# Optimization experiments

Measured on AMD Instinct MI355X. Metric: run time of the kernel, lower is better.

Reference implementation:

```python
import jax, jax.numpy as jnp
import numpy as np

NUM_USER = 200000
NUM_ITEM = 100000
DIM_E = 64
N_LAYERS = 3
N_INTER = 1000000  # raw sampled interactions (deduped below)
BATCH = 8192
EDGE_DROP = 0.5    # torch uses np.random.random()*1.0; fixed here for determinism
TGT_DROP = 0.5     # self.dropout


def _xavier_uniform(key, shape):
    fan_in, fan_out = shape[0], shape[1]
    b = np.sqrt(6.0 / (fan_in + fan_out)).astype(np.float32)
    return jax.random.uniform(key, shape, jnp.float32, -b, b)


def setup_inputs() -> dict:
    rng = np.random.default_rng(0)
    u = rng.integers(0, NUM_USER, N_INTER).astype(np.int64)
    it = rng.integers(0, NUM_ITEM, N_INTER).astype(np.int64)
    pair = np.unique(u * NUM_ITEM + it)  # dedupe like the dok_matrix update
    u, it = pair // NUM_ITEM, pair % NUM_ITEM
    # symmetric bipartite adjacency A over N = U + I nodes
    rows = np.concatenate([u, it + NUM_USER])
    cols = np.concatenate([it + NUM_USER, u])
    n_nodes = NUM_USER + NUM_ITEM
    deg = np.bincount(rows, minlength=n_nodes).astype(np.float32) + 1e-7
    dinv = np.power(deg, -0.5)
    vals = (dinv[rows] * dinv[cols]).astype(np.float32)  # D^-1/2 A D^-1/2

    key = jax.random.key(0)
    k1, k2, k3, k4 = jax.random.split(key, 4)
    return {
        "user_emb": _xavier_uniform(k1, (NUM_USER, DIM_E)),
        "item_emb": _xavier_uniform(k2, (NUM_ITEM, DIM_E)),
        "adj_vals": jnp.asarray(vals),
        "adj_rows": jnp.asarray(rows),
        "adj_cols": jnp.asarray(cols),
        "users": jax.random.randint(k3, (BATCH,), 0, NUM_USER),
        "items": jax.random.randint(k4, (BATCH,), 0, NUM_ITEM),
    }


def _spmm(rows, cols, vals, x, n_nodes):
    # out[r] = sum_e vals[e] * x[cols[e]] for rows[e] == r  (COO SpMM)
    return jax.ops.segment_sum(vals[:, None] * x[cols], rows, num_segments=n_nodes)


def reference(user_emb, item_emb, adj_vals, adj_rows, adj_cols, users, items):
    n_nodes = user_emb.shape[0] + item_emb.shape[0]
    kd = jax.random.key(1234)
    ke, ku, ki = jax.random.split(kd, 3)

    # sparse edge dropout: floor(1-rate + U[0,1)) keep mask, rescale by 1/(1-rate)
    keep = jnp.floor(1.0 - EDGE_DROP + jax.random.uniform(ke, adj_vals.shape))
    vals = adj_vals * keep * (1.0 / (1.0 - EDGE_DROP))

    x = jnp.concatenate([user_emb, item_emb], axis=0)  # [N, D]
    acc = x
    for _ in range(N_LAYERS):
        x = _spmm(adj_rows, adj_cols, vals, x, n_nodes)
        acc = acc + x
    all_emb = acc / (N_LAYERS + 1)  # mean over the stacked hops

    u_all = all_emb[:user_emb.shape[0]]
    i_all = all_emb[user_emb.shape[0]:]
    u_online = u_all[users]
    i_online = i_all[items]

    # targets: detached copies with standard dropout
    u_t = jax.lax.stop_gradient(u_online)
    i_t = jax.lax.stop_gradient(i_online)
    um = jax.random.bernoulli(ku, 1.0 - TGT_DROP, u_t.shape)
    im = jax.random.bernoulli(ki, 1.0 - TGT_DROP, i_t.shape)
    u_target = jnp.where(um, u_t / (1.0 - TGT_DROP), 0.0)
    i_target = jnp.where(im, i_t / (1.0 - TGT_DROP), 0.0)
    return (u_online, u_target, i_online, i_target)
```

## Files before the change

kernel.cpp:

```cpp
#include <hip/hip_runtime.h>
#include <stdint.h>

__host__ __device__ inline void tf2x32(uint32_t k0, uint32_t k1,
                                       uint32_t x0, uint32_t x1,
                                       uint32_t& o0, uint32_t& o1) {
  const uint32_t ks2 = k0 ^ k1 ^ 0x1BD11BDAu;
  x0 += k0; x1 += k1;
#define TFR(r) { x0 += x1; x1 = (x1 << (r)) | (x1 >> (32 - (r))); x1 ^= x0; }
  TFR(13) TFR(15) TFR(26) TFR(6)
  x0 += k1;  x1 += ks2 + 1u;
  TFR(17) TFR(29) TFR(16) TFR(24)
  x0 += ks2; x1 += k0 + 2u;
  TFR(13) TFR(15) TFR(26) TFR(6)
  x0 += k0;  x1 += k1 + 3u;
  TFR(17) TFR(29) TFR(16) TFR(24)
  x0 += k1;  x1 += ks2 + 4u;
  TFR(13) TFR(15) TFR(26) TFR(6)
  x0 += ks2; x1 += k0 + 5u;
#undef TFR
  o0 = x0; o1 = x1;
}

__host__ __device__ inline uint32_t bits32(uint32_t k0, uint32_t k1, uint32_t idx) {
  uint32_t a, b;
  tf2x32(k0, k1, 0u, idx, a, b);
  return a ^ b;
}

__device__ inline bool edge_kept(uint32_t k0, uint32_t k1, uint32_t e) {
  return (bits32(k0, k1, e) >> 31) != 0u;
}

__device__ inline float bf_lo(uint32_t u) { return __uint_as_float(u << 16); }
__device__ inline float bf_hi(uint32_t u) { return __uint_as_float(u & 0xffff0000u); }
__device__ inline uint32_t bf_pack(float a, float b) {
  uint32_t lo = (__float_as_uint(a) + 0x8000u) >> 16;
  uint32_t hi = (__float_as_uint(b) + 0x8000u) & 0xffff0000u;
  return hi | lo;
}

__device__ inline void fma8_f32(float a[8], float v, const float4& x0, const float4& x1) {
  a[0] = fmaf(v, x0.x, a[0]); a[1] = fmaf(v, x0.y, a[1]);
  a[2] = fmaf(v, x0.z, a[2]); a[3] = fmaf(v, x0.w, a[3]);
  a[4] = fmaf(v, x1.x, a[4]); a[5] = fmaf(v, x1.y, a[5]);
  a[6] = fmaf(v, x1.z, a[6]); a[7] = fmaf(v, x1.w, a[7]);
}
__device__ inline void fma8_bf(float a[8], float v, const uint4& u) {
  a[0] = fmaf(v, bf_lo(u.x), a[0]); a[1] = fmaf(v, bf_hi(u.x), a[1]);
  a[2] = fmaf(v, bf_lo(u.y), a[2]); a[3] = fmaf(v, bf_hi(u.y), a[3]);
  a[4] = fmaf(v, bf_lo(u.z), a[4]); a[5] = fmaf(v, bf_hi(u.z), a[5]);
  a[6] = fmaf(v, bf_lo(u.w), a[6]); a[7] = fmaf(v, bf_hi(u.w), a[7]);
}

__global__ __launch_bounds__(1024) void k_keep(
    const int* __restrict__ rows, int E, int E2, int nu,
    unsigned long long* __restrict__ keepw, int* __restrict__ bsumE,
    int* __restrict__ cnt, uint32_t ke0, uint32_t ke1) {
  __shared__ int s[16];
  int e = blockIdx.x * 1024 + threadIdx.x;
  int lane = threadIdx.x & 63;
  int wid = threadIdx.x >> 6;
  bool kept = (e < E) && edge_kept(ke0, ke1, (uint32_t)e);
  unsigned long long m = __ballot(kept);
  int ws = blockIdx.x * 1024 + wid * 64;
  if (lane == 0 && ws < E) keepw[ws >> 6] = m;
  int nf = 0;
  if (ws + 64 <= E2) nf = __popcll(m);
  else if (ws < E2) nf = __popcll(m & ((1ull << (E2 - ws)) - 1ull));
  if (lane == 0) s[wid] = nf;
  __syncthreads();
  if (threadIdx.x == 0) {
    int t = 0;
    for (int i = 0; i < 16; ++i) t += s[i];
    bsumE[blockIdx.x] = t;
  }
  if (kept && e >= E2) atomicAdd(&cnt[rows[e] - nu], 1);
}

__device__ inline void scan_block_1024(const int* __restrict__ bsum, int nb,
                                       int* __restrict__ bpref,
                                       int* a, int* b) {
  int t = threadIdx.x;
  for (int i = t; i < 2048; i += 1024) a[i] = (i < nb) ? bsum[i] : 0;
  __syncthreads();
  int* cur = a; int* nxt = b;
  for (int off = 1; off < 2048; off <<= 1) {
    for (int i = t; i < 2048; i += 1024)
      nxt[i] = cur[i] + (i >= off ? cur[i - off] : 0);
    __syncthreads();
    int* tmp = cur; cur = nxt; nxt = tmp;
  }
  for (int i = t; i <= nb; i += 1024)
    bpref[i] = (i == 0) ? 0 : cur[i - 1];
  __syncthreads();
}

__global__ void k_scanb2x(const int* __restrict__ bsumA, int nbA, int* __restrict__ bprefA,
                          const int* __restrict__ bsumB, int nbB, int* __restrict__ bprefB) {
  __shared__ int a[2048], b[2048];
  scan_block_1024(bsumA, nbA, bprefA, a, b);
  scan_block_1024(bsumB, nbB, bprefB, a, b);
}

__global__ void k_blocksum(const int* __restrict__ cnt, int n, int* __restrict__ bsum) {
  __shared__ int s[256];
  int i = blockIdx.x * 256 + threadIdx.x;
  s[threadIdx.x] = (i < n) ? cnt[i] : 0;
  __syncthreads();
  for (int off = 128; off > 0; off >>= 1) {
    if (threadIdx.x < off) s[threadIdx.x] += s[threadIdx.x + off];
    __syncthreads();
  }
  if (threadIdx.x == 0) bsum[blockIdx.x] = s[0];
}

__global__ void k_scan_write(const int* __restrict__ cnt, int n, const int* __restrict__ bpref,
                             int* __restrict__ row_ptr, int* __restrict__ nextc) {
  __shared__ int a[256], b[256];
  int t = threadIdx.x;
  int i = blockIdx.x * 256 + t;
  int v = (i < n) ? cnt[i] : 0;
  a[t] = v;
  __syncthreads();
  int* cur = a; int* nxt = b;
  for (int off = 1; off < 256; off <<= 1) {
    nxt[t] = cur[t] + (t >= off ? cur[t - off] : 0);
    __syncthreads();
    int* tmp = cur; cur = nxt; nxt = tmp;
  }
  int incl = cur[t] + bpref[blockIdx.x];
  int excl = incl - v;
  if (i < n) { row_ptr[i] = excl; nextc[i] = excl; }
  if (i == n - 1) row_ptr[n] = incl;
}

__global__ __launch_bounds__(1024) void k_compactU(
    const int* __restrict__ rows, const int* __restrict__ cols,
    const float* __restrict__ avals, const unsigned long long* __restrict__ keepw,
    const int* __restrict__ bprefE, int E2, int nu, int nbE,
    int2* __restrict__ uslot, int* __restrict__ row_ptr_u) {
  __shared__ int a[1024], b[1024];
  int t = threadIdx.x;
  int e = blockIdx.x * 1024 + t;
  bool kept = (e < E2) && ((keepw[e >> 6] >> (e & 63)) & 1ull);
  a[t] = kept ? 1 : 0;
  __syncthreads();
  int* cur = a; int* nxt = b;
  for (int off = 1; off < 1024; off <<= 1) {
    nxt[t] = cur[t] + (t >= off ? cur[t - off] : 0);
    __syncthreads();
    int* tmp = cur; cur = nxt; nxt = tmp;
  }
  int excl = cur[t] - (kept ? 1 : 0);
  int pos = bprefE[blockIdx.x] + excl;
  if (kept) uslot[pos] = make_int2(cols[e], __float_as_int(avals[e] * 2.0f));
  if (e < E2) {
    int r = rows[e];
    int rp = (e == 0) ? -1 : rows[e - 1];
    for (int rr = rp + 1; rr <= r; ++rr) row_ptr_u[rr] = pos;
    if (e == E2 - 1) {
      int total = bprefE[nbE];
      for (int rr = r + 1; rr <= nu; ++rr) row_ptr_u[rr] = total;
    }
  }
}

__global__ void k_scatterI(const int* __restrict__ rows, const int* __restrict__ cols,
                           const float* __restrict__ avals,
                           const unsigned long long* __restrict__ keepw,
                           int E, int E2, int nu, int* __restrict__ nextc,
                           int2* __restrict__ islot) {
  int e = E2 + blockIdx.x * 256 + threadIdx.x;
  if (e >= E) return;
  if (!((keepw[e >> 6] >> (e & 63)) & 1ull)) return;
  int r = rows[e] - nu;
  int k = atomicAdd(&nextc[r], 1);
  islot[k] = make_int2(cols[e], __float_as_int(avals[e] * 2.0f));
}

__global__ void k_mark_batch(const int* __restrict__ users, const int* __restrict__ items,
                             int batch, int nu, uint8_t* fB, uint8_t* f1, uint8_t* f2) {
  int i = blockIdx.x * 256 + threadIdx.x;
  if (i >= 2 * batch) return;
  int r = (i < batch) ? users[i] : nu + items[i - batch];
  fB[r] = 1; f1[r] = 1; f2[r] = 1;
}

__global__ void k_mark_neighbors(const uint8_t* __restrict__ fin,
                                 const int* __restrict__ row_ptr_u,
                                 const int2* __restrict__ uslot,
                                 const int* __restrict__ row_ptr_i,
                                 const int2* __restrict__ islot,
                                 int n, int nu, uint8_t* __restrict__ fout) {
  int r = blockIdx.x * 256 + threadIdx.x;
  if (r >= n) return;
  if (!fin[r]) return;
  const int* rp = (r < nu) ? row_ptr_u : row_ptr_i;
  const int2* sl = (r < nu) ? uslot : islot;
  int rr = (r < nu) ? r : r - nu;
  int s = rp[rr], e = rp[rr + 1];
  for (int k = s; k < e; ++k) fout[sl[k].x] = 1;
}

__global__ void k_flagsum2(const uint8_t* __restrict__ f1, const uint8_t* __restrict__ f2,
                           int n, int* __restrict__ bsum1, int* __restrict__ bsum2) {
  __shared__ int s1[256], s2[256];
  int i = blockIdx.x * 256 + threadIdx.x;
  s1[threadIdx.x] = (i < n) ? (int)f1[i] : 0;
  s2[threadIdx.x] = (i < n) ? (int)f2[i] : 0;
  __syncthreads();
  for (int off = 128; off > 0; off >>= 1) {
    if (threadIdx.x < off) {
      s1[threadIdx.x] += s1[threadIdx.x + off];
      s2[threadIdx.x] += s2[threadIdx.x + off];
    }
    __syncthreads();
  }
  if (threadIdx.x == 0) { bsum1[blockIdx.x] = s1[0]; bsum2[blockIdx.x] = s2[0]; }
}

__global__ void k_compact2(const uint8_t* __restrict__ f1, const uint8_t* __restrict__ f2,
                           int n, const int* __restrict__ bpref1,
                           const int* __restrict__ bpref2,
                           int* __restrict__ list1, int* __restrict__ list2) {
  __shared__ int a[256], b[256];
  int t = threadIdx.x;
  int i = blockIdx.x * 256 + t;

  int v = (i < n) ? (int)f1[i] : 0;
  a[t] = v;
  __syncthreads();
  int* cur = a; int* nxt = b;
  for (int off = 1; off < 256; off <<= 1) {
    nxt[t] = cur[t] + (t >= off ? cur[t - off] : 0);
    __syncthreads();
    int* tmp = cur; cur = nxt; nxt = tmp;
  }
  if (v) list1[bpref1[blockIdx.x] + cur[t] - 1] = i;
  __syncthreads();

  v = (i < n) ? (int)f2[i] : 0;
  a[t] = v;
  __syncthreads();
  cur = a; nxt = b;
  for (int off = 1; off < 256; off <<= 1) {
    nxt[t] = cur[t] + (t >= off ? cur[t - off] : 0);
    __syncthreads();
    int* tmp = cur; cur = nxt; nxt = tmp;
  }
  if (v) list2[bpref2[blockIdx.x] + cur[t] - 1] = i;
}

template <int FIRST>
__global__ __launch_bounds__(256) void k_spmm(
    const int* __restrict__ row_ptr_u, const int2* __restrict__ uslot,
    const int* __restrict__ row_ptr_i, const int2* __restrict__ islot,
    const uint32_t* __restrict__ xin, const float* __restrict__ uemb,
    const float* __restrict__ iemb, uint32_t* __restrict__ xout,
    const int* __restrict__ rowlist, const int* __restrict__ nrows_p, int nu) {
  int nrows = *nrows_p;
  int i = blockIdx.x * 32 + (threadIdx.x >> 3);
  if (i >= nrows) return;
  int r = rowlist[i];
  int j = threadIdx.x & 7;
  bool isu = r < nu;
  const int* rp = isu ? row_ptr_u : row_ptr_i;
  const int2* sl = isu ? uslot : islot;
  int rr = isu ? r : r - nu;
  int s = rp[rr], e = rp[rr + 1];
  float a[8] = {0, 0, 0, 0, 0, 0, 0, 0};
  int last = e - 1;
  for (int k = s; k < e; k += 4) {
    int i1 = (k + 1 <= last) ? k + 1 : last;
    int i2 = (k + 2 <= last) ? k + 2 : last;
    int i3 = (k + 3 <= last) ? k + 3 : last;
    int2 s0 = sl[k], s1 = sl[i1], s2 = sl[i2], s3 = sl[i3];
    float v0 = __int_as_float(s0.y);
    float v1 = (k + 1 <= last) ? __int_as_float(s1.y) : 0.0f;
    float v2 = (k + 2 <= last) ? __int_as_float(s2.y) : 0.0f;
    float v3 = (k + 3 <= last) ? __int_as_float(s3.y) : 0.0f;
    if (FIRST) {
      const float* p0 = (s0.x < nu) ? uemb + (size_t)s0.x * 64
                                    : iemb + (size_t)(s0.x - nu) * 64;
      const float* p1 = (s1.x < nu) ? uemb + (size_t)s1.x * 64
                                    : iemb + (size_t)(s1.x - nu) * 64;
      const float* p2 = (s2.x < nu) ? uemb + (size_t)s2.x * 64
                                    : iemb + (size_t)(s2.x - nu) * 64;
      const float* p3 = (s3.x < nu) ? uemb + (size_t)s3.x * 64
                                    : iemb + (size_t)(s3.x - nu) * 64;
      float4 xa0 = *(const float4*)(p0 + 8 * j);
      float4 xb0 = *(const float4*)(p0 + 8 * j + 4);
      float4 xa1 = *(const float4*)(p1 + 8 * j);
      float4 xb1 = *(const float4*)(p1 + 8 * j + 4);
      float4 xa2 = *(const float4*)(p2 + 8 * j);
      float4 xb2 = *(const float4*)(p2 + 8 * j + 4);
      float4 xa3 = *(const float4*)(p3 + 8 * j);
      float4 xb3 = *(const float4*)(p3 + 8 * j + 4);
      fma8_f32(a, v0, xa0, xb0);
      fma8_f32(a, v1, xa1, xb1);
      fma8_f32(a, v2, xa2, xb2);
      fma8_f32(a, v3, xa3, xb3);
    } else {
      uint4 u0 = *(const uint4*)(xin + (size_t)s0.x * 32 + 4 * j);
      uint4 u1 = *(const uint4*)(xin + (size_t)s1.x * 32 + 4 * j);
      uint4 u2 = *(const uint4*)(xin + (size_t)s2.x * 32 + 4 * j);
      uint4 u3 = *(const uint4*)(xin + (size_t)s3.x * 32 + 4 * j);
      fma8_bf(a, v0, u0);
      fma8_bf(a, v1, u1);
      fma8_bf(a, v2, u2);
      fma8_bf(a, v3, u3);
    }
  }
  uint4 o;
  o.x = bf_pack(a[0], a[1]); o.y = bf_pack(a[2], a[3]);
  o.z = bf_pack(a[4], a[5]); o.w = bf_pack(a[6], a[7]);
  *(uint4*)(xout + (size_t)r * 32 + 4 * j) = o;
}

__global__ void k_gatherA(const uint32_t* __restrict__ x0, const float* __restrict__ uemb,
                          const float* __restrict__ iemb, const int* __restrict__ users,
                          const int* __restrict__ items, float* __restrict__ out,
                          int batch, int nu) {
  int b = blockIdx.x * 32 + (threadIdx.x >> 3);
  if (b >= 2 * batch) return;
  int j = threadIdx.x & 7;
  size_t H = (size_t)batch * 64;
  int row; size_t dst; bool isu = b < batch;
  if (isu) {
    row = users[b];
    dst = (size_t)b * 64 + 8 * j;
  } else {
    int bi = b - batch;
    row = items[bi];
    dst = 2 * H + (size_t)bi * 64 + 8 * j;
  }
  const float* p = (isu ? uemb + (size_t)row * 64 : iemb + (size_t)row * 64) + 8 * j;
  float4 t0 = *(const float4*)p;
  float4 t1 = *(const float4*)(p + 4);
  int xr = isu ? row : nu + row;
  uint4 u = *(const uint4*)(x0 + (size_t)xr * 32 + 4 * j);
  t0.x += bf_lo(u.x); t0.y += bf_hi(u.x); t0.z += bf_lo(u.y); t0.w += bf_hi(u.y);
  t1.x += bf_lo(u.z); t1.y += bf_hi(u.z); t1.z += bf_lo(u.w); t1.w += bf_hi(u.w);
  *(float4*)(out + dst) = t0;
  *(float4*)(out + dst + 4) = t1;
}

__global__ __launch_bounds__(256) void k_tail(
    const int* __restrict__ row_ptr_u, const int2* __restrict__ uslot,
    const int* __restrict__ row_ptr_i, const int2* __restrict__ islot,
    const uint32_t* __restrict__ x1, const int* __restrict__ users,
    const int* __restrict__ items, float* __restrict__ out,
    int batch, int nu,
    uint32_t ku0, uint32_t ku1, uint32_t ki0, uint32_t ki1) {
  int b = blockIdx.x * 32 + (threadIdx.x >> 3);
  if (b >= 2 * batch) return;
  int j = threadIdx.x & 7;
  size_t H = (size_t)batch * 64;
  const int* rp; const int2* sl; int rr; size_t dst; int f0; uint32_t mk0, mk1;
  bool isu = b < batch;
  if (isu) {
    rr = users[b];
    rp = row_ptr_u; sl = uslot;
    dst = (size_t)b * 64 + 8 * j;
    f0 = b * 64 + 8 * j;
    mk0 = ku0; mk1 = ku1;
  } else {
    int bi = b - batch;
    rr = items[bi];
    rp = row_ptr_i; sl = islot;
    dst = 2 * H + (size_t)bi * 64 + 8 * j;
    f0 = bi * 64 + 8 * j;
    mk0 = ki0; mk1 = ki1;
  }
  int s = rp[rr], e = rp[rr + 1];
  float a[8] = {0, 0, 0, 0, 0, 0, 0, 0};
  int last = e - 1;
  for (int k = s; k < e; k += 4) {
    int i1 = (k + 1 <= last) ? k + 1 : last;
    int i2 = (k + 2 <= last) ? k + 2 : last;
    int i3 = (k + 3 <= last) ? k + 3 : last;
    int2 s0 = sl[k], s1 = sl[i1], s2 = sl[i2], s3 = sl[i3];
    float v0 = __int_as_float(s0.y);
    float v1 = (k + 1 <= last) ? __int_as_float(s1.y) : 0.0f;
    float v2 = (k + 2 <= last) ? __int_as_float(s2.y) : 0.0f;
    float v3 = (k + 3 <= last) ? __int_as_float(s3.y) : 0.0f;
    uint4 u0 = *(const uint4*)(x1 + (size_t)s0.x * 32 + 4 * j);
    uint4 u1 = *(const uint4*)(x1 + (size_t)s1.x * 32 + 4 * j);
    uint4 u2 = *(const uint4*)(x1 + (size_t)s2.x * 32 + 4 * j);
    uint4 u3 = *(const uint4*)(x1 + (size_t)s3.x * 32 + 4 * j);
    fma8_bf(a, v0, u0);
    fma8_bf(a, v1, u1);
    fma8_bf(a, v2, u2);
    fma8_bf(a, v3, u3);
  }
  int xr = isu ? rr : nu + rr;
  uint4 u = *(const uint4*)(x1 + (size_t)xr * 32 + 4 * j);
  float* o = out + dst;
  float4 t0 = *(float4*)o;
  float4 t1 = *(float4*)(o + 4);
  t0.x += bf_lo(u.x); t0.y += bf_hi(u.x); t0.z += bf_lo(u.y); t0.w += bf_hi(u.y);
  t1.x += bf_lo(u.z); t1.y += bf_hi(u.z); t1.z += bf_lo(u.w); t1.w += bf_hi(u.w);
  t0.x += a[0]; t0.y += a[1]; t0.z += a[2]; t0.w += a[3];
  t1.x += a[4]; t1.y += a[5]; t1.z += a[6]; t1.w += a[7];
  float ov[8] = {t0.x * 0.25f, t0.y * 0.25f, t0.z * 0.25f, t0.w * 0.25f,
                 t1.x * 0.25f, t1.y * 0.25f, t1.z * 0.25f, t1.w * 0.25f};
  float tv[8];
#pragma unroll
  for (int c = 0; c < 8; ++c) {
    bool present = (bits32(mk0, mk1, (uint32_t)(f0 + c)) >> 31) == 0u;
    tv[c] = present ? ov[c] * 2.0f : 0.0f;
  }
  *(float4*)o = make_float4(ov[0], ov[1], ov[2], ov[3]);
  *(float4*)(o + 4) = make_float4(ov[4], ov[5], ov[6], ov[7]);
  *(float4*)(o + H) = make_float4(tv[0], tv[1], tv[2], tv[3]);
  *(float4*)(o + H + 4) = make_float4(tv[4], tv[5], tv[6], tv[7]);
}

extern "C" void kernel_launch(void* const* d_in, const int* in_sizes, int n_in,
                              void* d_out, int out_size, void* d_ws, size_t ws_size,
                              hipStream_t stream) {
  const float* uemb  = (const float*)d_in[0];
  const float* iemb  = (const float*)d_in[1];
  const float* avals = (const float*)d_in[2];
  const int*   rows  = (const int*)d_in[3];
  const int*   cols  = (const int*)d_in[4];
  const int*   users = (const int*)d_in[5];
  const int*   items = (const int*)d_in[6];
  const int DIM = 64;
  const int NU = in_sizes[0] / DIM;
  const int NI = in_sizes[1] / DIM;
  const int E  = in_sizes[2];
  const int E2 = E / 2;
  const int B = in_sizes[5];
  const int NN = NU + NI;
  float* out = (float*)d_out;
  (void)n_in; (void)out_size; (void)ws_size;

  uint32_t ke0, ke1, ku0, ku1, ki0, ki1;
  tf2x32(0u, 1234u, 0u, 0u, ke0, ke1);
  tf2x32(0u, 1234u, 0u, 1u, ku0, ku1);
  tf2x32(0u, 1234u, 0u, 2u, ki0, ki1);

  char* p = (char*)d_ws;
  auto carve = [&](size_t bytes) {
    char* r = p;
    p += (bytes + 255) & ~(size_t)255;
    return (void*)r;
  };
  uint32_t* X0    = (uint32_t*)carve((size_t)NN * 32 * 4);
  uint32_t* X1    = (uint32_t*)carve((size_t)NN * 32 * 4);
  int2*  uslot    = (int2*)carve((size_t)E2 * 8);
  int2*  islot    = (int2*)carve((size_t)(E - E2) * 8);
  unsigned long long* keepw = (unsigned long long*)carve(((size_t)E / 64 + 2) * 8);
  int*   cnt      = (int*)carve((size_t)NI * 4);
  int*   row_ptr_u = (int*)carve((size_t)(NU + 1) * 4);
  int*   row_ptr_i = (int*)carve((size_t)(NI + 1) * 4);
  int*   nextc    = (int*)carve((size_t)NI * 4);
  uint8_t* fB     = (uint8_t*)carve((size_t)NN * 3);
  uint8_t* f1     = fB + NN;
  uint8_t* f2     = fB + 2 * (size_t)NN;
  int*   list1    = (int*)carve((size_t)NN * 4);
  int*   list2    = (int*)carve((size_t)NN * 4);
  const int GK    = (E + 1023) / 1024;
  const int NBE   = (E2 + 1023) / 1024;
  const int NBI   = (NI + 255) / 256;
  const int NB    = (NN + 255) / 256;
  int*   bsumE    = (int*)carve((size_t)GK * 4);
  int*   bprefE   = (int*)carve((size_t)(NBE + 1) * 4);
  int*   bsumI    = (int*)carve((size_t)NBI * 4);
  int*   bprefI   = (int*)carve((size_t)(NBI + 1) * 4);
  int*   bsum1    = (int*)carve((size_t)NB * 4);
  int*   bpref1   = (int*)carve((size_t)(NB + 1) * 4);
  int*   bsum2    = (int*)carve((size_t)NB * 4);
  int*   bpref2   = (int*)carve((size_t)(NB + 1) * 4);

  hipMemsetAsync(cnt, 0, (size_t)NI * 4, stream);
  hipMemsetAsync(fB, 0, (size_t)NN * 3, stream);

  k_keep<<<GK, 1024, 0, stream>>>(rows, E, E2, NU, keepw, bsumE, cnt, ke0, ke1);
  k_blocksum<<<NBI, 256, 0, stream>>>(cnt, NI, bsumI);
  k_scanb2x<<<1, 1024, 0, stream>>>(bsumE, NBE, bprefE, bsumI, NBI, bprefI);
  k_scan_write<<<NBI, 256, 0, stream>>>(cnt, NI, bprefI, row_ptr_i, nextc);
  k_compactU<<<NBE, 1024, 0, stream>>>(rows, cols, avals, keepw, bprefE, E2, NU, NBE,
                                       uslot, row_ptr_u);
  {
    const int gI = (E - E2 + 255) / 256;
    k_scatterI<<<gI, 256, 0, stream>>>(rows, cols, avals, keepw, E, E2, NU, nextc, islot);
  }

  const int gB = (2 * B + 255) / 256;
  const int gN = (NN + 255) / 256;
  k_mark_batch<<<gB, 256, 0, stream>>>(users, items, B, NU, fB, f1, f2);
  k_mark_neighbors<<<gN, 256, 0, stream>>>(fB, row_ptr_u, uslot, row_ptr_i, islot, NN, NU, f2);
  k_mark_neighbors<<<gN, 256, 0, stream>>>(f2, row_ptr_u, uslot, row_ptr_i, islot, NN, NU, f1);
  k_flagsum2<<<NB, 256, 0, stream>>>(f1, f2, NN, bsum1, bsum2);
  k_scanb2x<<<1, 1024, 0, stream>>>(bsum1, NB, bpref1, bsum2, NB, bpref2);
  k_compact2<<<NB, 256, 0, stream>>>(f1, f2, NN, bpref1, bpref2, list1, list2);

  const int gG = (2 * B + 31) / 32;
  const int gS = (NN + 31) / 32;

  k_spmm<1><<<gS, 256, 0, stream>>>(row_ptr_u, uslot, row_ptr_i, islot, X1,
                                    uemb, iemb, X0, list1, bpref1 + NB, NU);
  k_gatherA<<<gG, 256, 0, stream>>>(X0, uemb, iemb, users, items, out, B, NU);
  k_spmm<0><<<gS, 256, 0, stream>>>(row_ptr_u, uslot, row_ptr_i, islot, X0,
                                    uemb, iemb, X1, list2, bpref2 + NB, NU);
  k_tail<<<gG, 256, 0, stream>>>(row_ptr_u, uslot, row_ptr_i, islot, X1,
                                 users, items, out, B, NU, ku0, ku1, ki0, ki1);
}
```

Before: 161.1 us.

## Unify CSR, sort active rows by degree, fuse batch marking into keep kernel

Merges the user and item CSR arrays into one row_ptr/slot pair so kernels no longer branch on node type. Active-row lists now store (row, start, end) and are partitioned into small-degree and large-degree groups, which should balance the SpMM workgroups and skip row_ptr lookups. Batch marking is folded into the keep kernel, which removes one launch. Feature loads in the SpMM and output kernels change from 8 contiguous floats per lane to two 16-byte chunks split across the row halves, for more coalesced access. In exchange the row lists grow to 16 bytes per entry, and there is an extra scan and extra compaction passes.

Result: slower. 172.8 us (+7.2%).

```diff
diff --git a/kernel.cpp b/kernel.cpp
--- a/kernel.cpp
+++ b/kernel.cpp
@@ -52,10 +52,14 @@
   a[6] = fmaf(v, bf_lo(u.w), a[6]); a[7] = fmaf(v, bf_hi(u.w), a[7]);
 }
 
+#define SMALLMAX 4
+
 __global__ __launch_bounds__(1024) void k_keep(
     const int* __restrict__ rows, int E, int E2, int nu,
     unsigned long long* __restrict__ keepw, int* __restrict__ bsumE,
-    int* __restrict__ cnt, uint32_t ke0, uint32_t ke1) {
+    int* __restrict__ cnt, const int* __restrict__ users,
+    const int* __restrict__ items, int batch,
+    uint8_t* fB, uint8_t* f1, uint8_t* f2, uint32_t ke0, uint32_t ke1) {
   __shared__ int s[16];
   int e = blockIdx.x * 1024 + threadIdx.x;
   int lane = threadIdx.x & 63;
@@ -75,6 +79,10 @@
     bsumE[blockIdx.x] = t;
   }
   if (kept && e >= E2) atomicAdd(&cnt[rows[e] - nu], 1);
+  if (e < 2 * batch) {
+    int r = (e < batch) ? users[e] : nu + items[e - batch];
+    fB[r] = 1; f1[r] = 1; f2[r] = 1;
+  }
 }
 
 __device__ inline void scan_block_1024(const int* __restrict__ bsum, int nb,
@@ -95,11 +103,22 @@
   __syncthreads();
 }
 
-__global__ void k_scanb2x(const int* __restrict__ bsumA, int nbA, int* __restrict__ bprefA,
-                          const int* __restrict__ bsumB, int nbB, int* __restrict__ bprefB) {
+__global__ void k_scanb2x(const int* __restrict__ bA, int nA, int* __restrict__ pA,
+                          const int* __restrict__ bB, int nB, int* __restrict__ pB) {
   __shared__ int a[2048], b[2048];
-  scan_block_1024(bsumA, nbA, bprefA, a, b);
-  scan_block_1024(bsumB, nbB, bprefB, a, b);
+  scan_block_1024(bA, nA, pA, a, b);
+  scan_block_1024(bB, nB, pB, a, b);
+}
+
+__global__ void k_scanb4(const int* __restrict__ b1, int* __restrict__ p1,
+                         const int* __restrict__ b2, int* __restrict__ p2,
+                         const int* __restrict__ b3, int* __restrict__ p3,
+                         const int* __restrict__ b4, int* __restrict__ p4, int nb) {
+  __shared__ int a[2048], b[2048];
+  scan_block_1024(b1, nb, p1, a, b);
+  scan_block_1024(b2, nb, p2, a, b);
+  scan_block_1024(b3, nb, p3, a, b);
+  scan_block_1024(b4, nb, p4, a, b);
 }
 
 __global__ void k_blocksum(const int* __restrict__ cnt, int n, int* __restrict__ bsum) {
@@ -115,7 +134,8 @@
 }
 
 __global__ void k_scan_write(const int* __restrict__ cnt, int n, const int* __restrict__ bpref,
-                             int* __restrict__ row_ptr, int* __restrict__ nextc) {
+                             const int* __restrict__ basep,
+                             int* __restrict__ row_ptr_i, int* __restrict__ nextc) {
   __shared__ int a[256], b[256];
   int t = threadIdx.x;
   int i = blockIdx.x * 256 + t;
@@ -128,17 +148,18 @@
     __syncthreads();
     int* tmp = cur; cur = nxt; nxt = tmp;
   }
-  int incl = cur[t] + bpref[blockIdx.x];
+  int base = *basep;
+  int incl = cur[t] + bpref[blockIdx.x] + base;
   int excl = incl - v;
-  if (i < n) { row_ptr[i] = excl; nextc[i] = excl; }
-  if (i == n - 1) row_ptr[n] = incl;
+  if (i < n) { row_ptr_i[i] = excl; nextc[i] = excl; }
+  if (i == n - 1) row_ptr_i[n] = incl;
 }
 
 __global__ __launch_bounds__(1024) void k_compactU(
     const int* __restrict__ rows, const int* __restrict__ cols,
     const float* __restrict__ avals, const unsigned long long* __restrict__ keepw,
     const int* __restrict__ bprefE, int E2, int nu, int nbE,
-    int2* __restrict__ uslot, int* __restrict__ row_ptr_u) {
+    int2* __restrict__ slot, int* __restrict__ row_ptr) {
   __shared__ int a[1024], b[1024];
   int t = threadIdx.x;
   int e = blockIdx.x * 1024 + t;
@@ -153,14 +174,14 @@
   }
   int excl = cur[t] - (kept ? 1 : 0);
   int pos = bprefE[blockIdx.x] + excl;
-  if (kept) uslot[pos] = make_int2(cols[e], __float_as_int(avals[e] * 2.0f));
+  if (kept) slot[pos] = make_int2(cols[e], __float_as_int(avals[e] * 2.0f));
   if (e < E2) {
     int r = rows[e];
     int rp = (e == 0) ? -1 : rows[e - 1];
-    for (int rr = rp + 1; rr <= r; ++rr) row_ptr_u[rr] = pos;
+    for (int rr = rp + 1; rr <= r; ++rr) row_ptr[rr] = pos;
     if (e == E2 - 1) {
       int total = bprefE[nbE];
-      for (int rr = r + 1; rr <= nu; ++rr) row_ptr_u[rr] = total;
+      for (int rr = r + 1; rr <= nu; ++rr) row_ptr[rr] = total;
     }
   }
 }
@@ -169,66 +190,61 @@
                            const float* __restrict__ avals,
                            const unsigned long long* __restrict__ keepw,
                            int E, int E2, int nu, int* __restrict__ nextc,
-                           int2* __restrict__ islot) {
+                           int2* __restrict__ slot) {
   int e = E2 + blockIdx.x * 256 + threadIdx.x;
   if (e >= E) return;
   if (!((keepw[e >> 6] >> (e & 63)) & 1ull)) return;
   int r = rows[e] - nu;
   int k = atomicAdd(&nextc[r], 1);
-  islot[k] = make_int2(cols[e], __float_as_int(avals[e] * 2.0f));
-}
-
-__global__ void k_mark_batch(const int* __restrict__ users, const int* __restrict__ items,
-                             int batch, int nu, uint8_t* fB, uint8_t* f1, uint8_t* f2) {
-  int i = blockIdx.x * 256 + threadIdx.x;
-  if (i >= 2 * batch) return;
-  int r = (i < batch) ? users[i] : nu + items[i - batch];
-  fB[r] = 1; f1[r] = 1; f2[r] = 1;
+  slot[k] = make_int2(cols[e], __float_as_int(avals[e] * 2.0f));
 }
 
 __global__ void k_mark_neighbors(const uint8_t* __restrict__ fin,
-                                 const int* __restrict__ row_ptr_u,
-                                 const int2* __restrict__ uslot,
-                                 const int* __restrict__ row_ptr_i,
-                                 const int2* __restrict__ islot,
-                                 int n, int nu, uint8_t* __restrict__ fout) {
+                                 const int* __restrict__ row_ptr,
+                                 const int2* __restrict__ slot, int n,
+                                 uint8_t* __restrict__ fout) {
   int r = blockIdx.x * 256 + threadIdx.x;
   if (r >= n) return;
   if (!fin[r]) return;
-  const int* rp = (r < nu) ? row_ptr_u : row_ptr_i;
-  const int2* sl = (r < nu) ? uslot : islot;
-  int rr = (r < nu) ? r : r - nu;
-  int s = rp[rr], e = rp[rr + 1];
-  for (int k = s; k < e; ++k) fout[sl[k].x] = 1;
-}
-
-__global__ void k_flagsum2(const uint8_t* __restrict__ f1, const uint8_t* __restrict__ f2,
-                           int n, int* __restrict__ bsum1, int* __restrict__ bsum2) {
-  __shared__ int s1[256], s2[256];
-  int i = blockIdx.x * 256 + threadIdx.x;
-  s1[threadIdx.x] = (i < n) ? (int)f1[i] : 0;
-  s2[threadIdx.x] = (i < n) ? (int)f2[i] : 0;
+  int s = row_ptr[r], e = row_ptr[r + 1];
+  for (int k = s; k < e; ++k) fout[slot[k].x] = 1;
+}
+
+__global__ void k_flagsum4(const uint8_t* __restrict__ f1, const uint8_t* __restrict__ f2,
+                           const int* __restrict__ row_ptr, int n,
+                           int* __restrict__ bs1, int* __restrict__ bb1,
+                           int* __restrict__ bs2, int* __restrict__ bb2) {
+  __shared__ int h0[256], h1[256], h2[256], h3[256];
+  int t = threadIdx.x;
+  int i = blockIdx.x * 256 + t;
+  int deg = 0; bool a1 = false, a2 = false;
+  if (i < n) {
+    int s = row_ptr[i], e = row_ptr[i + 1];
+    deg = e - s;
+    a1 = f1[i]; a2 = f2[i];
+  }
+  bool sm = deg <= SMALLMAX;
+  h0[t] = (a1 && sm) ? 1 : 0; h1[t] = (a1 && !sm) ? 1 : 0;
+  h2[t] = (a2 && sm) ? 1 : 0; h3[t] = (a2 && !sm) ? 1 : 0;
   __syncthreads();
   for (int off = 128; off > 0; off >>= 1) {
-    if (threadIdx.x < off) {
-      s1[threadIdx.x] += s1[threadIdx.x + off];
-      s2[threadIdx.x] += s2[threadIdx.x + off];
+    if (t < off) {
+      h0[t] += h0[t + off]; h1[t] += h1[t + off];
+      h2[t] += h2[t + off]; h3[t] += h3[t + off];
     }
     __syncthreads();
   }
-  if (threadIdx.x == 0) { bsum1[blockIdx.x] = s1[0]; bsum2[blockIdx.x] = s2[0]; }
-}
-
-__global__ void k_compact2(const uint8_t* __restrict__ f1, const uint8_t* __restrict__ f2,
-                           int n, const int* __restrict__ bpref1,
-                           const int* __restrict__ bpref2,
-                           int* __restrict__ list1, int* __restrict__ list2) {
-  __shared__ int a[256], b[256];
+  if (t == 0) {
+    bs1[blockIdx.x] = h0[0]; bb1[blockIdx.x] = h1[0];
+    bs2[blockIdx.x] = h2[0]; bb2[blockIdx.x] = h3[0];
+  }
+}
+
+__device__ inline void emit_pass(bool flag, int r, int s, int e,
+                                 const int* __restrict__ bpref, int base0,
+                                 int4* __restrict__ list, int* a, int* b) {
   int t = threadIdx.x;
-  int i = blockIdx.x * 256 + t;
-
-  int v = (i < n) ? (int)f1[i] : 0;
-  a[t] = v;
+  a[t] = flag ? 1 : 0;
   __syncthreads();
   int* cur = a; int* nxt = b;
   for (int off = 1; off < 256; off <<= 1) {
@@ -236,45 +252,48 @@
     __syncthreads();
     int* tmp = cur; cur = nxt; nxt = tmp;
   }
-  if (v) list1[bpref1[blockIdx.x] + cur[t] - 1] = i;
-  __syncthreads();
-
-  v = (i < n) ? (int)f2[i] : 0;
-  a[t] = v;
-  __syncthreads();
-  cur = a; nxt = b;
-  for (int off = 1; off < 256; off <<= 1) {
-    nxt[t] = cur[t] + (t >= off ? cur[t - off] : 0);
-    __syncthreads();
-    int* tmp = cur; cur = nxt; nxt = tmp;
-  }
-  if (v) list2[bpref2[blockIdx.x] + cur[t] - 1] = i;
+  if (flag) list[base0 + bpref[blockIdx.x] + cur[t] - 1] = make_int4(r, s, e, 0);
+  __syncthreads();
+}
+
+__global__ void k_compact4(const uint8_t* __restrict__ f1, const uint8_t* __restrict__ f2,
+                           const int* __restrict__ row_ptr, int n, int nb,
+                           const int* __restrict__ ps1, const int* __restrict__ pb1,
+                           const int* __restrict__ ps2, const int* __restrict__ pb2,
+                           int4* __restrict__ list1, int4* __restrict__ list2) {
+  __shared__ int a[256], b[256];
+  int i = blockIdx.x * 256 + threadIdx.x;
+  int s = 0, e = 0; bool a1 = false, a2 = false;
+  if (i < n) {
+    s = row_ptr[i]; e = row_ptr[i + 1];
+    a1 = f1[i]; a2 = f2[i];
+  }
+  bool sm = (e - s) <= SMALLMAX;
+  emit_pass(a1 && sm, i, s, e, ps1, 0, list1, a, b);
+  emit_pass(a1 && !sm, i, s, e, pb1, ps1[nb], list1, a, b);
+  emit_pass(a2 && sm, i, s, e, ps2, 0, list2, a, b);
+  emit_pass(a2 && !sm, i, s, e, pb2, ps2[nb], list2, a, b);
 }
 
 template <int FIRST>
 __global__ __launch_bounds__(256) void k_spmm(
-    const int* __restrict__ row_ptr_u, const int2* __restrict__ uslot,
-    const int* __restrict__ row_ptr_i, const int2* __restrict__ islot,
-    const uint32_t* __restrict__ xin, const float* __restrict__ uemb,
-    const float* __restrict__ iemb, uint32_t* __restrict__ xout,
-    const int* __restrict__ rowlist, const int* __restrict__ nrows_p, int nu) {
-  int nrows = *nrows_p;
+    const int2* __restrict__ slot, const uint32_t* __restrict__ xin,
+    const float* __restrict__ uemb, const float* __restrict__ iemb,
+    uint32_t* __restrict__ xout, const int4* __restrict__ list,
+    const int* __restrict__ nsp, const int* __restrict__ nbp, int nu) {
+  int nrows = *nsp + *nbp;
   int i = blockIdx.x * 32 + (threadIdx.x >> 3);
   if (i >= nrows) return;
-  int r = rowlist[i];
+  int4 ent = list[i];
+  int r = ent.x, s = ent.y, e = ent.z;
   int j = threadIdx.x & 7;
-  bool isu = r < nu;
-  const int* rp = isu ? row_ptr_u : row_ptr_i;
-  const int2* sl = isu ? uslot : islot;
-  int rr = isu ? r : r - nu;
-  int s = rp[rr], e = rp[rr + 1];
   float a[8] = {0, 0, 0, 0, 0, 0, 0, 0};
   int last = e - 1;
   for (int k = s; k < e; k += 4) {
     int i1 = (k + 1 <= last) ? k + 1 : last;
     int i2 = (k + 2 <= last) ? k + 2 : last;
     int i3 = (k + 3 <= last) ? k + 3 : last;
-    int2 s0 = sl[k], s1 = sl[i1], s2 = sl[i2], s3 = sl[i3];
+    int2 s0 = slot[k], s1 = slot[i1], s2 = slot[i2], s3 = slot[i3];
     float v0 = __int_as_float(s0.y);
     float v1 = (k + 1 <= last) ? __int_as_float(s1.y) : 0.0f;
     float v2 = (k + 2 <= last) ? __int_as_float(s2.y) : 0.0f;
@@ -288,14 +307,14 @@
                                     : iemb + (size_t)(s2.x - nu) * 64;
       const float* p3 = (s3.x < nu) ? uemb + (size_t)s3.x * 64
                                     : iemb + (size_t)(s3.x - nu) * 64;
-      float4 xa0 = *(const float4*)(p0 + 8 * j);
-      float4 xb0 = *(const float4*)(p0 + 8 * j + 4);
-      float4 xa1 = *(const float4*)(p1 + 8 * j);
-      float4 xb1 = *(const float4*)(p1 + 8 * j + 4);
-      float4 xa2 = *(const float4*)(p2 + 8 * j);
-      float4 xb2 = *(const float4*)(p2 + 8 * j + 4);
-      float4 xa3 = *(const float4*)(p3 + 8 * j);
-      float4 xb3 = *(const float4*)(p3 + 8 * j + 4);
+      float4 xa0 = *(const float4*)(p0 + 4 * j);
+      float4 xb0 = *(const float4*)(p0 + 32 + 4 * j);
+      float4 xa1 = *(const float4*)(p1 + 4 * j);
+      float4 xb1 = *(const float4*)(p1 + 32 + 4 * j);
+      float4 xa2 = *(const float4*)(p2 + 4 * j);
+      float4 xb2 = *(const float4*)(p2 + 32 + 4 * j);
+      float4 xa3 = *(const float4*)(p3 + 4 * j);
+      float4 xb3 = *(const float4*)(p3 + 32 + 4 * j);
       fma8_f32(a, v0, xa0, xb0);
       fma8_f32(a, v1, xa1, xb1);
       fma8_f32(a, v2, xa2, xb2);
@@ -328,26 +347,25 @@
   int row; size_t dst; bool isu = b < batch;
   if (isu) {
     row = users[b];
-    dst = (size_t)b * 64 + 8 * j;
+    dst = (size_t)b * 64;
   } else {
     int bi = b - batch;
     row = items[bi];
-    dst = 2 * H + (size_t)bi * 64 + 8 * j;
-  }
-  const float* p = (isu ? uemb + (size_t)row * 64 : iemb + (size_t)row * 64) + 8 * j;
-  float4 t0 = *(const float4*)p;
-  float4 t1 = *(const float4*)(p + 4);
+    dst = 2 * H + (size_t)bi * 64;
+  }
+  const float* p = isu ? uemb + (size_t)row * 64 : iemb + (size_t)row * 64;
+  float4 t0 = *(const float4*)(p + 4 * j);
+  float4 t1 = *(const float4*)(p + 32 + 4 * j);
   int xr = isu ? row : nu + row;
   uint4 u = *(const uint4*)(x0 + (size_t)xr * 32 + 4 * j);
   t0.x += bf_lo(u.x); t0.y += bf_hi(u.x); t0.z += bf_lo(u.y); t0.w += bf_hi(u.y);
   t1.x += bf_lo(u.z); t1.y += bf_hi(u.z); t1.z += bf_lo(u.w); t1.w += bf_hi(u.w);
-  *(float4*)(out + dst) = t0;
-  *(float4*)(out + dst + 4) = t1;
+  *(float4*)(out + dst + 4 * j) = t0;
+  *(float4*)(out + dst + 32 + 4 * j) = t1;
 }
 
 __global__ __launch_bounds__(256) void k_tail(
-    const int* __restrict__ row_ptr_u, const int2* __restrict__ uslot,
-    const int* __restrict__ row_ptr_i, const int2* __restrict__ islot,
+    const int* __restrict__ row_ptr, const int2* __restrict__ slot,
     const uint32_t* __restrict__ x1, const int* __restrict__ users,
     const int* __restrict__ items, float* __restrict__ out,
     int batch, int nu,
@@ -356,30 +374,28 @@
   if (b >= 2 * batch) return;
   int j = threadIdx.x & 7;
   size_t H = (size_t)batch * 64;
-  const int* rp; const int2* sl; int rr; size_t dst; int f0; uint32_t mk0, mk1;
+  int rr; size_t dst; int fbase; uint32_t mk0, mk1;
   bool isu = b < batch;
   if (isu) {
     rr = users[b];
-    rp = row_ptr_u; sl = uslot;
-    dst = (size_t)b * 64 + 8 * j;
-    f0 = b * 64 + 8 * j;
+    dst = (size_t)b * 64;
+    fbase = b * 64;
     mk0 = ku0; mk1 = ku1;
   } else {
     int bi = b - batch;
-    rr = items[bi];
-    rp = row_ptr_i; sl = islot;
-    dst = 2 * H + (size_t)bi * 64 + 8 * j;
-    f0 = bi * 64 + 8 * j;
+    rr = nu + items[bi];
+    dst = 2 * H + (size_t)bi * 64;
+    fbase = (b - batch) * 64;
     mk0 = ki0; mk1 = ki1;
   }
-  int s = rp[rr], e = rp[rr + 1];
+  int s = row_ptr[rr], e = row_ptr[rr + 1];
   float a[8] = {0, 0, 0, 0, 0, 0, 0, 0};
   int last = e - 1;
   for (int k = s; k < e; k += 4) {
     int i1 = (k + 1 <= last) ? k + 1 : last;
     int i2 = (k + 2 <= last) ? k + 2 : last;
     int i3 = (k + 3 <= last) ? k + 3 : last;
-    int2 s0 = sl[k], s1 = sl[i1], s2 = sl[i2], s3 = sl[i3];
+    int2 s0 = slot[k], s1 = slot[i1], s2 = slot[i2], s3 = slot[i3];
     float v0 = __int_as_float(s0.y);
     float v1 = (k + 1 <= last) ? __int_as_float(s1.y) : 0.0f;
     float v2 = (k + 2 <= last) ? __int_as_float(s2.y) : 0.0f;
@@ -393,11 +409,11 @@
     fma8_bf(a, v2, u2);
     fma8_bf(a, v3, u3);
   }
-  int xr = isu ? rr : nu + rr;
-  uint4 u = *(const uint4*)(x1 + (size_t)xr * 32 + 4 * j);
-  float* o = out + dst;
-  float4 t0 = *(float4*)o;
-  float4 t1 = *(float4*)(o + 4);
+  uint4 u = *(const uint4*)(x1 + (size_t)rr * 32 + 4 * j);
+  float* o1 = out + dst + 4 * j;
+  float* o2 = out + dst + 32 + 4 * j;
+  float4 t0 = *(float4*)o1;
+  float4 t1 = *(float4*)o2;
   t0.x += bf_lo(u.x); t0.y += bf_hi(u.x); t0.z += bf_lo(u.y); t0.w += bf_hi(u.y);
   t1.x += bf_lo(u.z); t1.y += bf_hi(u.z); t1.z += bf_lo(u.w); t1.w += bf_hi(u.w);
   t0.x += a[0]; t0.y += a[1]; t0.z += a[2]; t0.w += a[3];
@@ -407,13 +423,14 @@
   float tv[8];
 #pragma unroll
   for (int c = 0; c < 8; ++c) {
-    bool present = (bits32(mk0, mk1, (uint32_t)(f0 + c)) >> 31) == 0u;
+    int d = (c < 4) ? (4 * j + c) : (32 + 4 * j + (c - 4));
+    bool present = (bits32(mk0, mk1, (uint32_t)(fbase + d)) >> 31) == 0u;
     tv[c] = present ? ov[c] * 2.0f : 0.0f;
   }
-  *(float4*)o = make_float4(ov[0], ov[1], ov[2], ov[3]);
-  *(float4*)(o + 4) = make_float4(ov[4], ov[5], ov[6], ov[7]);
-  *(float4*)(o + H) = make_float4(tv[0], tv[1], tv[2], tv[3]);
-  *(float4*)(o + H + 4) = make_float4(tv[4], tv[5], tv[6], tv[7]);
+  *(float4*)o1 = make_float4(ov[0], ov[1], ov[2], ov[3]);
+  *(float4*)o2 = make_float4(ov[4], ov[5], ov[6], ov[7]);
+  *(float4*)(o1 + H) = make_float4(tv[0], tv[1], tv[2], tv[3]);
+  *(float4*)(o2 + H) = make_float4(tv[4], tv[5], tv[6], tv[7]);
 }
 
 extern "C" void kernel_launch(void* const* d_in, const int* in_sizes, int n_in,
@@ -449,18 +466,16 @@
   };
   uint32_t* X0    = (uint32_t*)carve((size_t)NN * 32 * 4);
   uint32_t* X1    = (uint32_t*)carve((size_t)NN * 32 * 4);
-  int2*  uslot    = (int2*)carve((size_t)E2 * 8);
-  int2*  islot    = (int2*)carve((size_t)(E - E2) * 8);
+  int2*  slot     = (int2*)carve((size_t)E * 8);
   unsigned long long* keepw = (unsigned long long*)carve(((size_t)E / 64 + 2) * 8);
   int*   cnt      = (int*)carve((size_t)NI * 4);
-  int*   row_ptr_u = (int*)carve((size_t)(NU + 1) * 4);
-  int*   row_ptr_i = (int*)carve((size_t)(NI + 1) * 4);
+  int*   row_ptr  = (int*)carve((size_t)(NN + 1) * 4);
   int*   nextc    = (int*)carve((size_t)NI * 4);
   uint8_t* fB     = (uint8_t*)carve((size_t)NN * 3);
   uint8_t* f1     = fB + NN;
   uint8_t* f2     = fB + 2 * (size_t)NN;
-  int*   list1    = (int*)carve((size_t)NN * 4);
-  int*   list2    = (int*)carve((size_t)NN * 4);
+  int4*  list1    = (int4*)carve((size_t)NN * 16);
+  int4*  list2    = (int4*)carve((size_t)NN * 16);
   const int GK    = (E + 1023) / 1024;
   const int NBE   = (E2 + 1023) / 1024;
   const int NBI   = (NI + 255) / 256;
@@ -469,42 +484,47 @@
   int*   bprefE   = (int*)carve((size_t)(NBE + 1) * 4);
   int*   bsumI    = (int*)carve((size_t)NBI * 4);
   int*   bprefI   = (int*)carve((size_t)(NBI + 1) * 4);
-  int*   bsum1    = (int*)carve((size_t)NB * 4);
-  int*   bpref1   = (int*)carve((size_t)(NB + 1) * 4);
-  int*   bsum2    = (int*)carve((size_t)NB * 4);
-  int*   bpref2   = (int*)carve((size_t)(NB + 1) * 4);
+  int*   bs1      = (int*)carve((size_t)NB * 4);
+  int*   bb1      = (int*)carve((size_t)NB * 4);
+  int*   bs2      = (int*)carve((size_t)NB * 4);
+  int*   bb2      = (int*)carve((size_t)NB * 4);
+  int*   ps1      = (int*)carve((size_t)(NB + 1) * 4);
+  int*   pb1      = (int*)carve((size_t)(NB + 1) * 4);
+  int*   ps2      = (int*)carve((size_t)(NB + 1) * 4);
+  int*   pb2      = (int*)carve((size_t)(NB + 1) * 4);
 
   hipMemsetAsync(cnt, 0, (size_t)NI * 4, stream);
   hipMemsetAsync(fB, 0, (size_t)NN * 3, stream);
 
-  k_keep<<<GK, 1024, 0, stream>>>(rows, E, E2, NU, keepw, bsumE, cnt, ke0, ke1);
+  k_keep<<<GK, 1024, 0, stream>>>(rows, E, E2, NU, keepw, bsumE, cnt,
+                                  users, items, B, fB, f1, f2, ke0, ke1);
   k_blocksum<<<NBI, 256, 0, stream>>>(cnt, NI, bsumI);
   k_scanb2x<<<1, 1024, 0, stream>>>(bsumE, NBE, bprefE, bsumI, NBI, bprefI);
-  k_scan_write<<<NBI, 256, 0, stream>>>(cnt, NI, bprefI, row_ptr_i, nextc);
+  k_scan_write<<<NBI, 256, 0, stream>>>(cnt, NI, bprefI, bprefE + NBE,
+                                        row_ptr + NU, nextc);
   k_compactU<<<NBE, 1024, 0, stream>>>(rows, cols, avals, keepw, bprefE, E2, NU, NBE,
-                                       uslot, row_ptr_u);
+                                       slot, row_ptr);
   {
     const int gI = (E - E2 + 255) / 256;
-    k_scatterI<<<gI, 256, 0, stream>>>(rows, cols, avals, keepw, E, E2, NU, nextc, islot);
-  }
-
-  const int gB = (2 * B + 255) / 256;
+    k_scatterI<<<gI, 256, 0, stream>>>(rows, cols, avals, keepw, E, E2, NU, nextc, slot);
+  }
+
   const int gN = (NN + 255) / 256;
-  k_mark_batch<<<gB, 256, 0, stream>>>(users, items, B, NU, fB, f1, f2);
-  k_mark_neighbors<<<gN, 256, 0, stream>>>(fB, row_ptr_u, uslot, row_ptr_i, islot, NN, NU, f2);
-  k_mark_neighbors<<<gN, 256, 0, stream>>>(f2, row_ptr_u, uslot, row_ptr_i, islot, NN, NU, f1);
-  k_flagsum2<<<NB, 256, 0, stream>>>(f1, f2, NN, bsum1, bsum2);
-  k_scanb2x<<<1, 1024, 0, stream>>>(bsum1, NB, bpref1, bsum2, NB, bpref2);
-  k_compact2<<<NB, 256, 0, stream>>>(f1, f2, NN, bpref1, bpref2, list1, list2);
+  k_mark_neighbors<<<gN, 256, 0, stream>>>(fB, row_ptr, slot, NN, f2);
+  k_mark_neighbors<<<gN, 256, 0, stream>>>(f2, row_ptr, slot, NN, f1);
+  k_flagsum4<<<NB, 256, 0, stream>>>(f1, f2, row_ptr, NN, bs1, bb1, bs2, bb2);
+  k_scanb4<<<1, 1024, 0, stream>>>(bs1, ps1, bb1, pb1, bs2, ps2, bb2, pb2, NB);
+  k_compact4<<<NB, 256, 0, stream>>>(f1, f2, row_ptr, NN, NB, ps1, pb1, ps2, pb2,
+                                     list1, list2);
 
   const int gG = (2 * B + 31) / 32;
   const int gS = (NN + 31) / 32;
 
-  k_spmm<1><<<gS, 256, 0, stream>>>(row_ptr_u, uslot, row_ptr_i, islot, X1,
-                                    uemb, iemb, X0, list1, bpref1 + NB, NU);
+  k_spmm<1><<<gS, 256, 0, stream>>>(slot, X1, uemb, iemb, X0, list1,
+                                    ps1 + NB, pb1 + NB, NU);
   k_gatherA<<<gG, 256, 0, stream>>>(X0, uemb, iemb, users, items, out, B, NU);
-  k_spmm<0><<<gS, 256, 0, stream>>>(row_ptr_u, uslot, row_ptr_i, islot, X0,
-                                    uemb, iemb, X1, list2, bpref2 + NB, NU);
-  k_tail<<<gG, 256, 0, stream>>>(row_ptr_u, uslot, row_ptr_i, islot, X1,
-                                 users, items, out, B, NU, ku0, ku1, ki0, ki1);
-}
+  k_spmm<0><<<gS, 256, 0, stream>>>(slot, X0, uemb, iemb, X1, list2,
+                                    ps2 + NB, pb2 + NB, NU);
+  k_tail<<<gG, 256, 0, stream>>>(row_ptr, slot, X1, users, items, out, B, NU,
+                                 ku0, ku1, ki0, ki1);
+}
```
